# Kernel optimization log

Measured on AMD Instinct MI355X. Metric: run time of the kernel, lower is better.

The kernel has to match this reference:

```python
import jax, jax.numpy as jnp
import numpy as np
from jax import lax

B, CIN, COUT, H, W = 4, 256, 128, 64, 64
K, KK, PAD = 3, 9, 1
DK, DS, DP = 4, 2, 1  # deconv kernel/stride/pad
EPS = 1e-5


def setup_inputs() -> dict:
    key = jax.random.key(0)
    ks = jax.random.split(key, 6)
    x = jax.random.normal(ks[0], (B, CIN, H, W), jnp.float32)
    w_off = jax.random.normal(ks[1], (3 * KK, CIN, K, K), jnp.float32) * 0.01
    b_off = jnp.zeros((3 * KK,), jnp.float32)
    w_dcn = jax.random.normal(ks[2], (COUT, CIN, K, K), jnp.float32) / np.float32(np.sqrt(CIN * KK))
    b_dcn = jnp.zeros((COUT,), jnp.float32)
    gamma1 = jnp.ones((COUT,), jnp.float32)
    beta1 = jnp.zeros((COUT,), jnp.float32)
    # torch ConvTranspose2d weight layout: [in_ch, out_ch, kh, kw]
    w_up = jax.random.normal(ks[3], (COUT, COUT, DK, DK), jnp.float32) / np.float32(np.sqrt(COUT * DK * DK))
    gamma2 = jnp.ones((COUT,), jnp.float32)
    beta2 = jnp.zeros((COUT,), jnp.float32)
    return dict(x=x, w_off=w_off, b_off=b_off, w_dcn=w_dcn, b_dcn=b_dcn,
                gamma1=gamma1, beta1=beta1, w_up=w_up, gamma2=gamma2, beta2=beta2)


def _conv3(x, w, b):
    y = lax.conv_general_dilated(x, w, window_strides=(1, 1), padding=[(PAD, PAD), (PAD, PAD)],
                                 dimension_numbers=('NCHW', 'OIHW', 'NCHW'))
    return y + b[None, :, None, None]


def _bn(x, g, b):
    m = x.mean((0, 2, 3), keepdims=True)
    v = x.var((0, 2, 3), keepdims=True)
    return g[None, :, None, None] * (x - m) * lax.rsqrt(v + EPS) + b[None, :, None, None]


def _mdcn(x, offset, mask, w, b):
    # x: [B,C,H,W]; offset: [B,2*KK,H,W] interleaved (y,x) per kernel pt; mask: [B,KK,H,W]
    Bn, C, Hh, Ww = x.shape
    off = offset.reshape(Bn, KK, 2, Hh, Ww)
    dy, dx = off[:, :, 0], off[:, :, 1]                      # [B,KK,H,W]
    ky, kx = jnp.meshgrid(jnp.arange(K), jnp.arange(K), indexing='ij')
    ky = ky.reshape(KK).astype(x.dtype)
    kx = kx.reshape(KK).astype(x.dtype)
    ys = jnp.arange(Hh, dtype=x.dtype)[None, None, :, None] - PAD + ky[None, :, None, None] + dy
    xs = jnp.arange(Ww, dtype=x.dtype)[None, None, None, :] - PAD + kx[None, :, None, None] + dx
    y0f = jnp.floor(ys); x0f = jnp.floor(xs)
    ly = ys - y0f; lx = xs - x0f                              # fractional parts [B,KK,H,W]
    y0 = y0f.astype(jnp.int32); x0 = x0f.astype(jnp.int32)

    def gather(img, yi, xi):  # img [C,H,W], yi/xi [KK,H,W] -> [C,KK,H,W], zero out-of-bounds
        valid = ((yi >= 0) & (yi < Hh) & (xi >= 0) & (xi < Ww)).astype(img.dtype)
        v = img[:, jnp.clip(yi, 0, Hh - 1), jnp.clip(xi, 0, Ww - 1)]
        return v * valid[None]

    g = jax.vmap(gather)
    v00 = g(x, y0, x0)
    v01 = g(x, y0, x0 + 1)
    v10 = g(x, y0 + 1, x0)
    v11 = g(x, y0 + 1, x0 + 1)                                # [B,C,KK,H,W]
    val = (v00 * ((1 - ly) * (1 - lx))[:, None] + v01 * ((1 - ly) * lx)[:, None]
           + v10 * (ly * (1 - lx))[:, None] + v11 * (ly * lx)[:, None])
    val = val * mask[:, None]
    out = jnp.einsum('bckhw,ock->bohw', val, w.reshape(w.shape[0], C, KK))
    return out + b[None, :, None, None]


def _deconv(x, w_up):
    # torch ConvTranspose2d(k=DK, s=DS, p=DP) == fractionally strided conv with flipped kernel
    w = jnp.flip(jnp.transpose(w_up, (1, 0, 2, 3)), (2, 3))   # [out,in,kh,kw]
    p = DK - 1 - DP
    return lax.conv_general_dilated(x, w, window_strides=(1, 1), padding=[(p, p), (p, p)],
                                    lhs_dilation=(DS, DS), dimension_numbers=('NCHW', 'OIHW', 'NCHW'))


def reference(x, w_off, b_off, w_dcn, b_dcn, gamma1, beta1, w_up, gamma2, beta2):
    om = _conv3(x, w_off, b_off)                              # [B,27,H,W]
    o1, o2, m = jnp.split(om, 3, axis=1)
    offset = jnp.concatenate([o1, o2], axis=1)                # [B,18,H,W]
    mask = jax.nn.sigmoid(m)                                  # [B,9,H,W]
    y = _mdcn(x, offset, mask, w_dcn, b_dcn)                  # [B,COUT,H,W]
    y = jax.nn.relu(_bn(y, gamma1, beta1))
    y = _deconv(y, w_up)                                      # [B,COUT,2H,2W]
    y = jax.nn.relu(_bn(y, gamma2, beta2))
    return y
```

## Files before the change

### kernel.cpp

```cpp
#include <hip/hip_runtime.h>
#include <hip/hip_bf16.h>

typedef __attribute__((ext_vector_type(8))) short short8;
typedef __attribute__((ext_vector_type(4))) float f32x4;
typedef __attribute__((ext_vector_type(16))) float f32x16;
typedef unsigned short u16;
typedef unsigned int u32;

#define OFF_XT      0u
#define OFF_OM      8388608u
#define OFF_Y       10485760u
#define OFF_Y2      14680064u
#define OFF_BOFF    31457280u
#define OFF_BDCN    31604736u
#define OFF_BUP     32194560u
#define OFF_STATS   32718848u

__device__ __forceinline__ float lo2f(u32 u){ u32 v = u << 16; float f; __builtin_memcpy(&f, &v, 4); return f; }
__device__ __forceinline__ float hi2f(u32 u){ u32 v = u & 0xffff0000u; float f; __builtin_memcpy(&f, &v, 4); return f; }
__device__ __forceinline__ float b2f(u16 v){ u32 u = ((u32)v) << 16; float f; __builtin_memcpy(&f, &u, 4); return f; }
__device__ __forceinline__ u16 f2b(float f){ __hip_bfloat16 h = __float2bfloat16(f); u16 r; __builtin_memcpy(&r, &h, 2); return r; }
__device__ __forceinline__ u32 rne(float f){ u32 u; __builtin_memcpy(&u, &f, 4); return u + 0x7FFFu + ((u >> 16) & 1u); }
__device__ __forceinline__ u32 pk2(float f0, float f1){ return (rne(f0) >> 16) | (rne(f1) & 0xFFFF0000u); }

__device__ __forceinline__ f32x4 mfma16(short8 a, short8 b, f32x4 c){
  return __builtin_amdgcn_mfma_f32_16x16x32_bf16(a, b, c, 0, 0, 0);
}
__device__ __forceinline__ f32x16 mfma32(short8 a, short8 b, f32x16 c){
  return __builtin_amdgcn_mfma_f32_32x32x16_bf16(a, b, c, 0, 0, 0);
}
__device__ __forceinline__ void unpk(uint4 u, float* f){
  f[0]=lo2f(u.x); f[1]=hi2f(u.x); f[2]=lo2f(u.y); f[3]=hi2f(u.y);
  f[4]=lo2f(u.z); f[5]=hi2f(u.z); f[6]=lo2f(u.w); f[7]=hi2f(u.w);
}
__device__ __forceinline__ uint4 pk8(const float* f){
  uint4 r;
  r.x = pk2(f[0], f[1]); r.y = pk2(f[2], f[3]);
  r.z = pk2(f[4], f[5]); r.w = pk2(f[6], f[7]);
  return r;
}

__global__ __launch_bounds__(256) void prep_kernel(const float* __restrict__ w_off,
                                                   const float* __restrict__ w_dcn,
                                                   const float* __restrict__ w_up,
                                                   u16* __restrict__ Boff,
                                                   u16* __restrict__ Bdcn,
                                                   u16* __restrict__ Bup){
  int i = blockIdx.x * 256 + threadIdx.x;
  if (i < 72*2*64*8){
    int j = i & 7, lane = (i >> 3) & 63, nt = (i >> 9) & 1, kc = i >> 10;
    int n = nt*16 + (lane & 15);
    int k = kc*32 + ((lane >> 4) & 3)*8 + j, tap = k >> 8, c = k & 255;
    int ky = tap / 3, kx = tap - ky*3;
    u16 v = 0;
    if (n < 27) v = f2b(w_off[((n*256 + c)*3 + ky)*3 + kx]);
    Boff[i] = v;
  }
  if (i < 72*8*64*8){
    int j = i & 7, lane = (i >> 3) & 63, nt = (i >> 9) & 7, kc = i >> 12;
    int o = nt*16 + (lane & 15);
    int k = kc*32 + ((lane >> 4) & 3)*8 + j, tap = k >> 8, c = k & 255;
    int ky = tap / 3, kx = tap - ky*3;
    Bdcn[i] = f2b(w_dcn[((o*256 + c)*3 + ky)*3 + kx]);
  }
  if (i < 4*32*4*2*32*8){
    int j = i & 7, n = (i >> 3) & 31, kh = (i >> 8) & 1, a4 = (i >> 9) & 3;
    int kc = (i >> 11) & 31, pp = i >> 16;
    int k = kc*16 + kh*8 + j, tapd = k >> 7, c = k & 127;
    int o = a4*32 + n;
    int py = pp >> 1, px = pp & 1, dy = tapd >> 1, dx = tapd & 1;
    Bup[i] = f2b(w_up[((c*128 + o)*4 + (3-(py+2*dy)))*4 + (3-(px+2*dx))]);
  }
}

__global__ __launch_bounds__(256) void transpose_kernel(const float* __restrict__ x, u16* __restrict__ xt){
  __shared__ u16 Ls[64][65];
  int blk = blockIdx.x;
  int cb = blk & 3, h = (blk >> 2) & 63, b = blk >> 8;
  int t = threadIdx.x;
  int c0 = cb * 64;
  for (int i = 0; i < 16; i++){
    int idx = t + i*256;
    int c = idx >> 6, w = idx & 63;
    Ls[c][w] = f2b(x[((b*256 + c0 + c)*64 + h)*64 + w]);
  }
  __syncthreads();
  for (int i = 0; i < 16; i++){
    int idx = t + i*256;
    int w = idx >> 6, cc = idx & 63;
    xt[(((b*64 + h)*64 + w) << 8) + c0 + cc] = Ls[cc][w];
  }
}

__global__ __launch_bounds__(256, 8) void convoff_kernel(const u16* __restrict__ xt,
                                                         const u16* __restrict__ Boff,
                                                         const float* __restrict__ b_off,
                                                         float* __restrict__ om){
  __shared__ alignas(16) char smem[16896];
  u16* As0 = (u16*)smem;
  u16* As1 = (u16*)(smem + 8448);
  float* Ys = (float*)smem;
  int blk = blockIdx.x;
  int wt = blk & 3, h = (blk >> 2) & 63, b = blk >> 8;
  int w0 = wt * 16;
  int P0 = (b*64 + h)*64 + w0;
  int t = threadIdx.x;
  int wv = t >> 6, lane = t & 63;
  int ln = lane & 15, q4 = (lane >> 4) & 3;
  int spx = t >> 5, sc16a = t & 31;
  f32x4 acc[2];
  acc[0] = (f32x4){0.f,0.f,0.f,0.f};
  acc[1] = (f32x4){0.f,0.f,0.f,0.f};
  uint4 pf[2];

  {
    int ky = -1, kx = -1;
    #pragma unroll
    for (int it = 0; it < 2; it++){
      int px = spx + it*8;
      int y = h + ky, xw = w0 + px + kx;
      pf[it] = make_uint4(0,0,0,0);
      if ((u32)y < 64u && (u32)xw < 64u)
        pf[it] = *(const uint4*)(xt + (((b*64 + y)*64 + xw) << 8) + sc16a*8);
    }
    #pragma unroll
    for (int it = 0; it < 2; it++)
      *(uint4*)(As0 + (spx + it*8)*264 + sc16a*8) = pf[it];
  }
  __syncthreads();

  for (int tap = 0; tap < 9; tap++){
    const u16* cur = (tap & 1) ? As1 : As0;
    u16* nxt = (tap & 1) ? As0 : As1;
    if (tap < 8){
      int tn = tap + 1;
      int ky = tn/3 - 1, kx = tn - (tn/3)*3 - 1;
      #pragma unroll
      for (int it = 0; it < 2; it++){
        int px = spx + it*8;
        int y = h + ky, xw = w0 + px + kx;
        pf[it] = make_uint4(0,0,0,0);
        if ((u32)y < 64u && (u32)xw < 64u)
          pf[it] = *(const uint4*)(xt + (((b*64 + y)*64 + xw) << 8) + sc16a*8);
      }
    }
    #pragma unroll
    for (int q = 0; q < 2; q++){
      int kcl = wv*2 + q;
      int kcg = tap*8 + kcl;
      short8 a = *(const short8*)(cur + ln*264 + kcl*32 + q4*8);
      #pragma unroll
      for (int nt = 0; nt < 2; nt++){
        short8 bb = *(const short8*)(Boff + ((kcg*2 + nt)*64 + lane)*8);
        acc[nt] = mfma16(a, bb, acc[nt]);
      }
    }
    if (tap < 8){
      #pragma unroll
      for (int it = 0; it < 2; it++)
        *(uint4*)(nxt + (spx + it*8)*264 + sc16a*8) = pf[it];
    }
    __syncthreads();
  }
  #pragma unroll
  for (int nt = 0; nt < 2; nt++)
    #pragma unroll
    for (int r = 0; r < 4; r++)
      Ys[(wv*16 + q4*4 + r)*36 + nt*16 + ln] = acc[nt][r];
  __syncthreads();
  {
    int px = t >> 4, s = t & 15;
    #pragma unroll
    for (int half = 0; half < 2; half++){
      int n = s + half*16;
      if (n < 27){
        float sum = Ys[(px)*36 + n] + Ys[(16 + px)*36 + n]
                  + Ys[(32 + px)*36 + n] + Ys[(48 + px)*36 + n] + b_off[n];
        om[(P0 + px)*32 + n] = sum;
      }
    }
  }
}

__global__ __launch_bounds__(256, 4) void mdcn_kernel(const u16* __restrict__ xt,
                                                      const float* __restrict__ om,
                                                      const u16* __restrict__ Bdcn,
                                                      const float* __restrict__ b_dcn,
                                                      u16* __restrict__ yb){
  __shared__ alignas(16) char smem[21504];
  u16* As0 = (u16*)smem;
  u16* As1 = (u16*)(smem + 8448);
  float* Ptab = (float*)(smem + 16896);
  u16* Lp = (u16*)(smem + 8448);
  int blk = blockIdx.x;
  int wt = blk & 3, h = (blk >> 2) & 63, b = blk >> 8;
  int w0 = wt * 16;
  int P0 = (b*64 + h)*64 + w0;
  int t = threadIdx.x;
  int wv = t >> 6, lane = t & 63;
  int m = lane & 31, kh = lane >> 5;
  int ln = lane & 15, q4 = (lane >> 4) & 3;
  float bias0 = b_dcn[wv*32 + ln];
  float bias1 = b_dcn[wv*32 + 16 + ln];

  if (t < 144){
    int px = t / 9, tap = t - (t/9)*9;
    int ky = tap / 3, kx = tap - ky*3;
    const float* omp = om + (P0 + px)*32;
    float dy  = omp[2*tap];
    float dxv = omp[2*tap + 1];
    float mk  = 1.f / (1.f + __expf(-omp[18 + tap]));
    float ys = (float)(h - 1 + ky) + dy;
    float xs = (float)(w0 + px - 1 + kx) + dxv;
    float y0f = floorf(ys), x0f = floorf(xs);
    float ly = ys - y0f, lx = xs - x0f;
    int y0 = (int)y0f, x0 = (int)x0f;
    bool vy0 = (u32)y0 < 64u, vy1 = (u32)(y0+1) < 64u;
    bool vx0 = (u32)x0 < 64u, vx1 = (u32)(x0+1) < 64u;
    int ya = min(max(y0, 0), 63),   ybr_ = min(max(y0+1, 0), 63);
    int xa = min(max(x0, 0), 63),   xb = min(max(x0+1, 0), 63);
    u32 a00 = (u32)(((b*64 + ya)*64 + xa) << 8);
    u32 a01 = (u32)(((b*64 + ya)*64 + xb) << 8);
    u32 a10 = (u32)(((b*64 + ybr_)*64 + xa) << 8);
    u32 a11 = (u32)(((b*64 + ybr_)*64 + xb) << 8);
    float w00 = (vy0 && vx0) ? (1.f-ly)*(1.f-lx)*mk : 0.f;
    float w01 = (vy0 && vx1) ? (1.f-ly)*lx*mk       : 0.f;
    float w10 = (vy1 && vx0) ? ly*(1.f-lx)*mk       : 0.f;
    float w11 = (vy1 && vx1) ? ly*lx*mk             : 0.f;
    float* P = Ptab + t*8;
    ((u32*)P)[0] = a00; ((u32*)P)[1] = a01; ((u32*)P)[2] = a10; ((u32*)P)[3] = a11;
    P[4] = w00; P[5] = w01; P[6] = w10; P[7] = w11;
  }
  __syncthreads();

  f32x4 acc[2];
  acc[0] = (f32x4){0.f,0.f,0.f,0.f};
  acc[1] = (f32x4){0.f,0.f,0.f,0.f};
  uint4 pu[8];
  float4 pwv[2];

  auto prefetch = [&](int tap){
    #pragma unroll
    for (int i = 0; i < 2; i++){
      int p = wv*4 + i*2 + kh;
      const float* P = Ptab + (p*9 + tap)*8;
      uint4 pa = *(const uint4*)P;
      pwv[i] = *(const float4*)(P + 4);
      pu[i*4+0] = *(const uint4*)(xt + pa.x + m*8);
      pu[i*4+1] = *(const uint4*)(xt + pa.y + m*8);
      pu[i*4+2] = *(const uint4*)(xt + pa.z + m*8);
      pu[i*4+3] = *(const uint4*)(xt + pa.w + m*8);
    }
  };
  auto blend_write = [&](u16* dst){
    #pragma unroll
    for (int i = 0; i < 2; i++){
      int p = wv*4 + i*2 + kh;
      float f00[8], f01[8], f10[8], f11[8], s[8];
      unpk(pu[i*4+0], f00); unpk(pu[i*4+1], f01);
      unpk(pu[i*4+2], f10); unpk(pu[i*4+3], f11);
      float4 w = pwv[i];
      #pragma unroll
      for (int j = 0; j < 8; j++)
        s[j] = w.x*f00[j] + w.y*f01[j] + w.z*f10[j] + w.w*f11[j];
      *(uint4*)(dst + p*264 + m*8) = pk8(s);
    }
  };

  prefetch(0);
  blend_write(As0);
  __syncthreads();

  for (int tap = 0; tap < 9; tap++){
    const u16* cur = (tap & 1) ? As1 : As0;
    u16* nxt = (tap & 1) ? As0 : As1;
    if (tap < 8) prefetch(tap + 1);
    {
      int nt0 = wv*2, nt1 = wv*2 + 1;
      int kcg0 = tap*8;
      short8 b0n = *(const short8*)(Bdcn + ((kcg0*8 + nt0)*64 + lane)*8);
      short8 b1n = *(const short8*)(Bdcn + ((kcg0*8 + nt1)*64 + lane)*8);
      #pragma unroll
      for (int kc = 0; kc < 8; kc++){
        short8 b0 = b0n, b1 = b1n;
        if (kc < 7){
          int kcg = tap*8 + kc + 1;
          b0n = *(const short8*)(Bdcn + ((kcg*8 + nt0)*64 + lane)*8);
          b1n = *(const short8*)(Bdcn + ((kcg*8 + nt1)*64 + lane)*8);
        }
        short8 a = *(const short8*)(cur + ln*264 + kc*32 + q4*8);
        acc[0] = mfma16(a, b0, acc[0]);
        acc[1] = mfma16(a, b1, acc[1]);
      }
    }
    if (tap < 8) blend_write(nxt);
    __syncthreads();
  }
  #pragma unroll
  for (int nt2 = 0; nt2 < 2; nt2++){
    int ch = wv*32 + nt2*16 + ln;
    float bias = nt2 ? bias1 : bias0;
    #pragma unroll
    for (int r = 0; r < 4; r++){
      int px = q4*4 + r;
      Lp[px*136 + ch] = (u16)(rne(acc[nt2][r] + bias) >> 16);
    }
  }
  __syncthreads();
  {
    int px = t >> 4, cg = t & 15;
    uint4 u = *(const uint4*)(Lp + px*136 + cg*8);
    *(uint4*)(yb + (P0 + px)*128 + cg*8) = u;
  }
}

__global__ __launch_bounds__(256) void bnstats_kernel(const u16* __restrict__ src,
                                                      float* __restrict__ st, int npix){
  __shared__ float red[256];
  int t = threadIdx.x;
  int ch = t & 127, half = t >> 7;
  float s = 0.f, ss = 0.f;
  for (int p = blockIdx.x*2 + half; p < npix; p += gridDim.x*2){
    float v = b2f(src[p*128 + ch]);
    s += v; ss += v*v;
  }
  red[t] = s; __syncthreads();
  if (t < 128) atomicAdd(&st[t], red[t] + red[t+128]);
  __syncthreads();
  red[t] = ss; __syncthreads();
  if (t < 128) atomicAdd(&st[128 + t], red[t] + red[t+128]);
}

__global__ __launch_bounds__(256) void bnstats_nchw_kernel(const u16* __restrict__ y2n,
                                                           float* __restrict__ st){
  __shared__ float red[8];
  int ch = blockIdx.x;
  int t = threadIdx.x;
  int wv = t >> 6, lane = t & 63;
  float s = 0.f, ss = 0.f;
  for (int b = 0; b < 4; b++){
    const u16* base = y2n + (((b*128 + ch) << 14)) + t*8;
    #pragma unroll
    for (int it = 0; it < 8; it++){
      uint4 u = *(const uint4*)(base + it*2048);
      float f[8]; unpk(u, f);
      #pragma unroll
      for (int e = 0; e < 8; e++){ s += f[e]; ss += f[e]*f[e]; }
    }
  }
  #pragma unroll
  for (int o = 32; o >= 1; o >>= 1){
    s  += __shfl_xor(s, o);
    ss += __shfl_xor(ss, o);
  }
  if (lane == 0){ red[wv*2] = s; red[wv*2+1] = ss; }
  __syncthreads();
  if (t == 0) st[ch]       = red[0] + red[2] + red[4] + red[6];
  if (t == 1) st[128 + ch] = red[1] + red[3] + red[5] + red[7];
}

__global__ __launch_bounds__(256, 6) void deconv_kernel(const u16* __restrict__ yb,
                                                        const float* __restrict__ stats1,
                                                        const float* __restrict__ gamma1,
                                                        const float* __restrict__ beta1,
                                                        const u16* __restrict__ Bup,
                                                        u16* __restrict__ y2n){
  __shared__ alignas(16) char smem[19520];
  u16* Ls = (u16*)smem;
  u16* Lo = (u16*)smem;
  float2* bnL = (float2*)(smem + 18496);
  int blk = blockIdx.x;
  int half = blk & 1, yy = (blk >> 1) & 127, b = blk >> 8;
  int pary = yy & 1;
  int hs = (yy - 2 + pary) >> 1;
  int X0 = half * 64, wbase = half*32 - 1;
  int t = threadIdx.x;
  if (t < 128){
    float mean = stats1[t] * (1.f/16384.f);
    float var  = stats1[128 + t] * (1.f/16384.f) - mean*mean;
    float inv  = rsqrtf(var + 1e-5f);
    float sc   = gamma1[t] * inv;
    bnL[t] = make_float2(sc, beta1[t] - mean * sc);
  }
  __syncthreads();
  #pragma unroll
  for (int it = 0; it < 5; it++){
    int idx = it*256 + t;
    if (idx < 1088){
      int r = idx / 544, rem = idx - r*544;
      int cc = rem >> 4, c16 = rem & 15;
      int hh = hs + r, w_in = wbase + cc;
      uint4 u = make_uint4(0,0,0,0);
      if ((u32)hh < 64u && (u32)w_in < 64u)
        u = *(const uint4*)(yb + (((b*64 + hh)*64 + w_in) << 7) + c16*8);
      float f[8]; unpk(u, f);
      float o[8];
      #pragma unroll
      for (int e = 0; e < 8; e++){
        float2 sc = bnL[c16*8 + e];
        o[e] = fmaxf(0.f, fmaf(sc.x, f[e], sc.y));
      }
      *(uint4*)(Ls + (r*34 + cc)*136 + c16*8) = pk8(o);
    }
  }
  __syncthreads();

  int wv = t >> 6, lane = t & 63;
  int m = lane & 31, kh = lane >> 5;
  int parx = wv & 1, nh = wv >> 1;
  int pp = pary*2 + parx;
  f32x16 acc[2];
  acc[0] = (f32x16){0.f};
  acc[1] = (f32x16){0.f};

  #pragma unroll
  for (int tapd = 0; tapd < 4; tapd++){
    int dyy = tapd >> 1, dxx = tapd & 1;
    const u16* lp = Ls + ((dyy*34 + m + parx + dxx)*136);
    #pragma unroll
    for (int q = 0; q < 8; q++){
      short8 a = *(const short8*)(lp + q*16 + kh*8);
      #pragma unroll
      for (int nt2 = 0; nt2 < 2; nt2++){
        int a4 = nh*2 + nt2;
        short8 bb = *(const short8*)(Bup + ((((pp*32 + tapd*8 + q)*4 + a4)*2 + kh)*32 + m)*8);
        acc[nt2] = mfma32(a, bb, acc[nt2]);
      }
    }
  }
  __syncthreads();
  #pragma unroll
  for (int nt2 = 0; nt2 < 2; nt2++){
    int ch = (nh*2 + nt2)*32 + m;
    #pragma unroll
    for (int r = 0; r < 16; r++){
      int mrow = (r & 3) + 8*(r >> 2) + 4*kh;
      int xl = parx + 2*mrow;
      Lo[xl*136 + ch] = (u16)(rne(acc[nt2][r]) >> 16);
    }
  }
  __syncthreads();
  {
    int ch = t >> 1, xh = t & 1;
    u16* gp = y2n + ((b*128 + ch)*128 + yy)*128 + X0 + xh*32;
    #pragma unroll
    for (int g = 0; g < 4; g++){
      u32 r4[4];
      #pragma unroll
      for (int e = 0; e < 4; e++){
        u32 lo = Lo[(xh*32 + g*8 + 2*e)*136 + ch];
        u32 hi = Lo[(xh*32 + g*8 + 2*e + 1)*136 + ch];
        r4[e] = lo | (hi << 16);
      }
      *(uint4*)(gp + g*8) = make_uint4(r4[0], r4[1], r4[2], r4[3]);
    }
  }
}

__global__ __launch_bounds__(256) void final_kernel(const u16* __restrict__ y2n,
                                                    const float* __restrict__ stats2,
                                                    const float* __restrict__ gamma2,
                                                    const float* __restrict__ beta2,
                                                    float* __restrict__ outp){
  int gid = blockIdx.x*256 + threadIdx.x;
  int idx = gid * 8;
  int ch = (idx >> 14) & 127;
  float mean = stats2[ch] * (1.f/65536.f);
  float var  = stats2[128 + ch] * (1.f/65536.f) - mean*mean;
  float inv  = rsqrtf(var + 1e-5f);
  float scx  = gamma2[ch] * inv;
  float scy  = beta2[ch] - mean * scx;
  uint4 u = *(const uint4*)(y2n + idx);
  float f[8]; unpk(u, f);
  float4 o0, o1;
  o0.x = fmaxf(0.f, fmaf(scx, f[0], scy));
  o0.y = fmaxf(0.f, fmaf(scx, f[1], scy));
  o0.z = fmaxf(0.f, fmaf(scx, f[2], scy));
  o0.w = fmaxf(0.f, fmaf(scx, f[3], scy));
  o1.x = fmaxf(0.f, fmaf(scx, f[4], scy));
  o1.y = fmaxf(0.f, fmaf(scx, f[5], scy));
  o1.z = fmaxf(0.f, fmaf(scx, f[6], scy));
  o1.w = fmaxf(0.f, fmaf(scx, f[7], scy));
  *(float4*)(outp + idx)     = o0;
  *(float4*)(outp + idx + 4) = o1;
}

extern "C" void kernel_launch(void* const* d_in, const int* in_sizes, int n_in,
                              void* d_out, int out_size, void* d_ws, size_t ws_size,
                              hipStream_t stream) {
  const float* x      = (const float*)d_in[0];
  const float* w_off  = (const float*)d_in[1];
  const float* b_off  = (const float*)d_in[2];
  const float* w_dcn  = (const float*)d_in[3];
  const float* b_dcn  = (const float*)d_in[4];
  const float* gamma1 = (const float*)d_in[5];
  const float* beta1  = (const float*)d_in[6];
  const float* w_up   = (const float*)d_in[7];
  const float* gamma2 = (const float*)d_in[8];
  const float* beta2  = (const float*)d_in[9];

  char* ws = (char*)d_ws;
  u16*   xt    = (u16*)(ws + OFF_XT);
  float* om    = (float*)(ws + OFF_OM);
  u16*   yb    = (u16*)(ws + OFF_Y);
  u16*   y2n   = (u16*)(ws + OFF_Y2);
  u16*   Boff  = (u16*)(ws + OFF_BOFF);
  u16*   Bdcn  = (u16*)(ws + OFF_BDCN);
  u16*   Bup   = (u16*)(ws + OFF_BUP);
  float* stats = (float*)(ws + OFF_STATS);

  (void)hipMemsetAsync(stats, 0, 2048, stream);
  prep_kernel<<<1152, 256, 0, stream>>>(w_off, w_dcn, w_up, Boff, Bdcn, Bup);
  transpose_kernel<<<1024, 256, 0, stream>>>(x, xt);
  convoff_kernel<<<1024, 256, 0, stream>>>(xt, Boff, b_off, om);
  mdcn_kernel<<<1024, 256, 0, stream>>>(xt, om, Bdcn, b_dcn, yb);
  bnstats_kernel<<<256, 256, 0, stream>>>(yb, stats, 16384);
  deconv_kernel<<<1024, 256, 0, stream>>>(yb, stats, gamma1, beta1, Bup, y2n);
  bnstats_nchw_kernel<<<128, 256, 0, stream>>>(y2n, stats + 256);
  final_kernel<<<4096, 256, 0, stream>>>(y2n, stats + 256, gamma2, beta2, (float*)d_out);
}
```

Baseline: 194.3 us.

## Fuse BN1 statistics into mdcn epilogue and widen BN2 stats grid

The first BatchNorm's per-channel sum and sum-of-squares now come from the bf16 tile already staged in LDS at the end of the mdcn kernel. Each block adds its partials with atomics, which removes the separate bnstats kernel launch and its re-read of the intermediate. The second stats kernel now splits work across batch as well as channel, 512 blocks instead of 128, and combines the partials with atomicAdd instead of plain stores. This relies on the stats buffer being zeroed beforehand, which the existing memset does. The cost is atomic contention and a nondeterministic summation order.

```diff
diff --git a/kernel.cpp b/kernel.cpp
--- a/kernel.cpp
+++ b/kernel.cpp
@@ -186,7 +186,8 @@
                                                       const float* __restrict__ om,
                                                       const u16* __restrict__ Bdcn,
                                                       const float* __restrict__ b_dcn,
-                                                      u16* __restrict__ yb){
+                                                      u16* __restrict__ yb,
+                                                      float* __restrict__ stats1){
   __shared__ alignas(16) char smem[21504];
   u16* As0 = (u16*)smem;
   u16* As1 = (u16*)(smem + 8448);
@@ -312,41 +313,33 @@
     uint4 u = *(const uint4*)(Lp + px*136 + cg*8);
     *(uint4*)(yb + (P0 + px)*128 + cg*8) = u;
   }
-}
-
-__global__ __launch_bounds__(256) void bnstats_kernel(const u16* __restrict__ src,
-                                                      float* __restrict__ st, int npix){
-  __shared__ float red[256];
-  int t = threadIdx.x;
-  int ch = t & 127, half = t >> 7;
-  float s = 0.f, ss = 0.f;
-  for (int p = blockIdx.x*2 + half; p < npix; p += gridDim.x*2){
-    float v = b2f(src[p*128 + ch]);
-    s += v; ss += v*v;
-  }
-  red[t] = s; __syncthreads();
-  if (t < 128) atomicAdd(&st[t], red[t] + red[t+128]);
-  __syncthreads();
-  red[t] = ss; __syncthreads();
-  if (t < 128) atomicAdd(&st[128 + t], red[t] + red[t+128]);
+  if (t < 128){
+    float s = 0.f, ss = 0.f;
+    #pragma unroll
+    for (int px = 0; px < 16; px++){
+      float v = b2f(Lp[px*136 + t]);
+      s += v; ss = fmaf(v, v, ss);
+    }
+    atomicAdd(&stats1[t], s);
+    atomicAdd(&stats1[128 + t], ss);
+  }
 }
 
 __global__ __launch_bounds__(256) void bnstats_nchw_kernel(const u16* __restrict__ y2n,
                                                            float* __restrict__ st){
   __shared__ float red[8];
-  int ch = blockIdx.x;
+  int blk = blockIdx.x;
+  int ch = blk >> 2, b = blk & 3;
   int t = threadIdx.x;
   int wv = t >> 6, lane = t & 63;
   float s = 0.f, ss = 0.f;
-  for (int b = 0; b < 4; b++){
-    const u16* base = y2n + (((b*128 + ch) << 14)) + t*8;
-    #pragma unroll
-    for (int it = 0; it < 8; it++){
-      uint4 u = *(const uint4*)(base + it*2048);
-      float f[8]; unpk(u, f);
-      #pragma unroll
-      for (int e = 0; e < 8; e++){ s += f[e]; ss += f[e]*f[e]; }
-    }
+  const u16* base = y2n + (((b*128 + ch) << 14)) + t*8;
+  #pragma unroll
+  for (int it = 0; it < 8; it++){
+    uint4 u = *(const uint4*)(base + it*2048);
+    float f[8]; unpk(u, f);
+    #pragma unroll
+    for (int e = 0; e < 8; e++){ s += f[e]; ss = fmaf(f[e], f[e], ss); }
   }
   #pragma unroll
   for (int o = 32; o >= 1; o >>= 1){
@@ -355,8 +348,8 @@
   }
   if (lane == 0){ red[wv*2] = s; red[wv*2+1] = ss; }
   __syncthreads();
-  if (t == 0) st[ch]       = red[0] + red[2] + red[4] + red[6];
-  if (t == 1) st[128 + ch] = red[1] + red[3] + red[5] + red[7];
+  if (t == 0) atomicAdd(&st[ch],       red[0] + red[2] + red[4] + red[6]);
+  if (t == 1) atomicAdd(&st[128 + ch], red[1] + red[3] + red[5] + red[7]);
 }
 
 __global__ __launch_bounds__(256, 6) void deconv_kernel(const u16* __restrict__ yb,
@@ -513,9 +506,8 @@
   prep_kernel<<<1152, 256, 0, stream>>>(w_off, w_dcn, w_up, Boff, Bdcn, Bup);
   transpose_kernel<<<1024, 256, 0, stream>>>(x, xt);
   convoff_kernel<<<1024, 256, 0, stream>>>(xt, Boff, b_off, om);
-  mdcn_kernel<<<1024, 256, 0, stream>>>(xt, om, Bdcn, b_dcn, yb);
-  bnstats_kernel<<<256, 256, 0, stream>>>(yb, stats, 16384);
+  mdcn_kernel<<<1024, 256, 0, stream>>>(xt, om, Bdcn, b_dcn, yb, stats);
   deconv_kernel<<<1024, 256, 0, stream>>>(yb, stats, gamma1, beta1, Bup, y2n);
-  bnstats_nchw_kernel<<<128, 256, 0, stream>>>(y2n, stats + 256);
+  bnstats_nchw_kernel<<<512, 256, 0, stream>>>(y2n, stats + 256);
   final_kernel<<<4096, 256, 0, stream>>>(y2n, stats + 256, gamma2, beta2, (float*)d_out);
 }
```

After: 196.3 us. No clear change (+1.1%).
